# Kernel tuning notes

Measured on AMD Instinct MI355X. Metric: run time of the kernel, lower is better.

Reference implementation:

```python
import jax, jax.numpy as jnp
import numpy as np

BINS = 10


def setup_inputs() -> dict:
    key = jax.random.key(0)
    k1, k2 = jax.random.split(key)
    N, C = 4194304, 16
    inputs = jax.random.normal(k1, (N, C), dtype=jnp.float32)
    target = jax.random.randint(k2, (N,), 0, 2, dtype=jnp.int64)
    return {"inputs": inputs, "target": target}


def reference(inputs, target):
    N = inputs.shape[0]
    edges = jnp.arange(BINS + 1, dtype=inputs.dtype) / BINS  # [0, 0.1, ..., 1.0]

    # p_t = softmax(inputs)[i, target_i]
    logp = jax.nn.log_softmax(inputs, axis=1)
    p_t = jnp.take_along_axis(jnp.exp(logp), target[:, None], axis=1)[:, 0]

    # gradient norm g = |p_t - target| (detached in the original)
    g = jnp.abs(jax.lax.stop_gradient(p_t) - target.astype(inputs.dtype))

    # bin index: matches (g >= edges[i]) & (g < edges[i+1]); clip handles g == 1.0
    bin_idx = jnp.clip(jnp.searchsorted(edges, g, side="right") - 1, 0, BINS - 1)

    # per-bin counts via one scatter-add (replaces the per-bin CPU loop)
    counts = jax.ops.segment_sum(jnp.ones_like(g), bin_idx, num_segments=BINS)
    counts = jnp.maximum(counts, 1.0)  # occupied bins always have count >= 1

    # weights[i] = (N / bins) / num_in_bin(i)
    weights = (N / BINS) / counts[bin_idx]

    # weighted cross entropy, summed
    nll = -jnp.take_along_axis(logp, target[:, None], axis=1)[:, 0]
    return jnp.sum(nll * weights)
```

## Files before the change

kernel.cpp:

```cpp
#include <hip/hip_runtime.h>

#define BINS 10

__global__ __launch_bounds__(256) void ghm_main(const float* __restrict__ x,
                                                const int* __restrict__ tgt,
                                                double* __restrict__ g_sum,
                                                unsigned int* __restrict__ g_cnt,
                                                int n_rows) {
    __shared__ double s_sum[BINS];
    __shared__ unsigned int s_cnt[BINS];
    if (threadIdx.x < BINS) { s_sum[threadIdx.x] = 0.0; s_cnt[threadIdx.x] = 0u; }
    __syncthreads();

    const float edges[BINS + 1] = {0.0f, 0.1f, 0.2f, 0.3f, 0.4f, 0.5f,
                                   0.6f, 0.7f, 0.8f, 0.9f, 1.0f};

    double acc[BINS];
    unsigned int cnt[BINS];
#pragma unroll
    for (int k = 0; k < BINS; ++k) { acc[k] = 0.0; cnt[k] = 0u; }

    const int j = threadIdx.x & 3;
    const int quad = (blockIdx.x * blockDim.x + threadIdx.x) >> 2;
    const int quads_total = (gridDim.x * blockDim.x) >> 2;

    for (int row = quad; row < n_rows; row += quads_total) {
        const float4 v = ((const float4*)x)[row * 4 + j];

        float m = fmaxf(fmaxf(v.x, v.y), fmaxf(v.z, v.w));
        m = fmaxf(m, __shfl_xor(m, 1));
        m = fmaxf(m, __shfl_xor(m, 2));

        float s = expf(v.x - m) + expf(v.y - m) + expf(v.z - m) + expf(v.w - m);
        s += __shfl_xor(s, 1);
        s += __shfl_xor(s, 2);

        if (j == 0) {
            const int t = tgt[row];
            const float xt = (t == 0) ? v.x : ((t == 1) ? v.y : ((t == 2) ? v.z : v.w));
            const float logp = xt - m - logf(s);
            const float p = expf(logp);
            const float g = fabsf(p - (float)t);

            int b = 0;
#pragma unroll
            for (int k = 1; k <= BINS; ++k) b += (g >= edges[k]) ? 1 : 0;
            if (b > BINS - 1) b = BINS - 1;

            const double nll = (double)(-logp);
#pragma unroll
            for (int k = 0; k < BINS; ++k) {
                const bool h = (b == k);
                acc[k] += h ? nll : 0.0;
                cnt[k] += h ? 1u : 0u;
            }
        }
    }

#pragma unroll
    for (int k = 0; k < BINS; ++k) {
        if (cnt[k] != 0u) {
            atomicAdd(&s_cnt[k], cnt[k]);
            atomicAdd(&s_sum[k], acc[k]);
        }
    }
    __syncthreads();

    if (threadIdx.x < BINS) {
        if (s_cnt[threadIdx.x] != 0u) {
            atomicAdd(&g_cnt[threadIdx.x * 32], s_cnt[threadIdx.x]);
            atomicAdd(&g_sum[threadIdx.x * 16], s_sum[threadIdx.x]);
        }
    }
}

__global__ void ghm_final(const double* __restrict__ g_sum,
                          const unsigned int* __restrict__ g_cnt,
                          float* __restrict__ out, int n_rows) {
    if (threadIdx.x == 0 && blockIdx.x == 0) {
        const double scale = (double)n_rows / (double)BINS;
        double total = 0.0;
        for (int b = 0; b < BINS; ++b) {
            double c = (double)g_cnt[b * 32];
            if (c < 1.0) c = 1.0;
            total += g_sum[b * 16] / c;
        }
        out[0] = (float)(total * scale);
    }
}

extern "C" void kernel_launch(void* const* d_in, const int* in_sizes, int n_in,
                              void* d_out, int out_size, void* d_ws, size_t ws_size,
                              hipStream_t stream) {
    const float* x = (const float*)d_in[0];
    const int* tgt = (const int*)d_in[1];
    const int n_rows = in_sizes[1];

    double* g_sum = (double*)d_ws;
    unsigned int* g_cnt = (unsigned int*)((char*)d_ws + 2048);

    hipMemsetAsync(d_ws, 0, 4096, stream);

    const int block = 256;
    const int grid = 2048;
    ghm_main<<<grid, block, 0, stream>>>(x, tgt, g_sum, g_cnt, n_rows);
    ghm_final<<<1, 64, 0, stream>>>(g_sum, g_cnt, (float*)d_out, n_rows);
}
```

Measured before the change: 391.8 us.

## Fuse final reduction via last-block pattern, drop memset, use nontemporal loads

Replaces the memset, global atomics, and separate final kernel with per-block slot writes plus a device-wide done counter, so the last block to finish reduces all slots and writes the output. The input loads become nontemporal. This removes two extra launches and contention on the global atomics. In exchange it relies on a global counter being reset correctly and adds a serial tail reduction inside one block.

```diff
diff --git a/kernel.cpp b/kernel.cpp
--- a/kernel.cpp
+++ b/kernel.cpp
@@ -1,14 +1,22 @@
 #include <hip/hip_runtime.h>
 
 #define BINS 10
+#define GRID 2048
+#define BLOCK 256
 
-__global__ __launch_bounds__(256) void ghm_main(const float* __restrict__ x,
-                                                const int* __restrict__ tgt,
-                                                double* __restrict__ g_sum,
-                                                unsigned int* __restrict__ g_cnt,
-                                                int n_rows) {
+typedef float floatx4 __attribute__((ext_vector_type(4)));
+
+__device__ unsigned int done_ctr = 0;
+
+__global__ __launch_bounds__(BLOCK) void ghm_fused(const float* __restrict__ x,
+                                                   const int* __restrict__ tgt,
+                                                   double* __restrict__ slot_sum,
+                                                   unsigned int* __restrict__ slot_cnt,
+                                                   float* __restrict__ out,
+                                                   int n_rows) {
     __shared__ double s_sum[BINS];
     __shared__ unsigned int s_cnt[BINS];
+    __shared__ int s_last;
     if (threadIdx.x < BINS) { s_sum[threadIdx.x] = 0.0; s_cnt[threadIdx.x] = 0u; }
     __syncthreads();
 
@@ -21,23 +29,23 @@
     for (int k = 0; k < BINS; ++k) { acc[k] = 0.0; cnt[k] = 0u; }
 
     const int j = threadIdx.x & 3;
-    const int quad = (blockIdx.x * blockDim.x + threadIdx.x) >> 2;
-    const int quads_total = (gridDim.x * blockDim.x) >> 2;
+    const int quad = (blockIdx.x * BLOCK + threadIdx.x) >> 2;
+    const int quads_total = (GRID * BLOCK) >> 2;
 
     for (int row = quad; row < n_rows; row += quads_total) {
-        const float4 v = ((const float4*)x)[row * 4 + j];
+        const floatx4 v = __builtin_nontemporal_load(((const floatx4*)x) + (row * 4 + j));
 
-        float m = fmaxf(fmaxf(v.x, v.y), fmaxf(v.z, v.w));
+        float m = fmaxf(fmaxf(v[0], v[1]), fmaxf(v[2], v[3]));
         m = fmaxf(m, __shfl_xor(m, 1));
         m = fmaxf(m, __shfl_xor(m, 2));
 
-        float s = expf(v.x - m) + expf(v.y - m) + expf(v.z - m) + expf(v.w - m);
+        float s = expf(v[0] - m) + expf(v[1] - m) + expf(v[2] - m) + expf(v[3] - m);
         s += __shfl_xor(s, 1);
         s += __shfl_xor(s, 2);
 
         if (j == 0) {
             const int t = tgt[row];
-            const float xt = (t == 0) ? v.x : ((t == 1) ? v.y : ((t == 2) ? v.z : v.w));
+            const float xt = (t == 0) ? v[0] : ((t == 1) ? v[1] : ((t == 2) ? v[2] : v[3]));
             const float logp = xt - m - logf(s);
             const float p = expf(logp);
             const float g = fabsf(p - (float)t);
@@ -67,25 +75,58 @@
     __syncthreads();
 
     if (threadIdx.x < BINS) {
-        if (s_cnt[threadIdx.x] != 0u) {
-            atomicAdd(&g_cnt[threadIdx.x * 32], s_cnt[threadIdx.x]);
-            atomicAdd(&g_sum[threadIdx.x * 16], s_sum[threadIdx.x]);
+        slot_sum[threadIdx.x * GRID + blockIdx.x] = s_sum[threadIdx.x];
+        slot_cnt[threadIdx.x * GRID + blockIdx.x] = s_cnt[threadIdx.x];
+    }
+    __syncthreads();
+
+    if (threadIdx.x == 0) {
+        const unsigned int old =
+            __hip_atomic_fetch_add(&done_ctr, 1u, __ATOMIC_ACQ_REL, __HIP_MEMORY_SCOPE_AGENT);
+        s_last = (old == GRID - 1) ? 1 : 0;
+    }
+    __syncthreads();
+
+    if (s_last) {
+        double bsum[BINS];
+        unsigned int bcnt[BINS];
+#pragma unroll
+        for (int k = 0; k < BINS; ++k) { bsum[k] = 0.0; bcnt[k] = 0u; }
+        for (int i = threadIdx.x; i < GRID; i += BLOCK) {
+#pragma unroll
+            for (int k = 0; k < BINS; ++k) {
+                bsum[k] += slot_sum[k * GRID + i];
+                bcnt[k] += slot_cnt[k * GRID + i];
+            }
         }
-    }
-}
-
-__global__ void ghm_final(const double* __restrict__ g_sum,
-                          const unsigned int* __restrict__ g_cnt,
-                          float* __restrict__ out, int n_rows) {
-    if (threadIdx.x == 0 && blockIdx.x == 0) {
-        const double scale = (double)n_rows / (double)BINS;
-        double total = 0.0;
-        for (int b = 0; b < BINS; ++b) {
-            double c = (double)g_cnt[b * 32];
-            if (c < 1.0) c = 1.0;
-            total += g_sum[b * 16] / c;
+#pragma unroll
+        for (int k = 0; k < BINS; ++k) {
+            for (int off = 32; off > 0; off >>= 1) {
+                bsum[k] += __shfl_down(bsum[k], off);
+                bcnt[k] += __shfl_down(bcnt[k], off);
+            }
         }
-        out[0] = (float)(total * scale);
+        if (threadIdx.x < BINS) { s_sum[threadIdx.x] = 0.0; s_cnt[threadIdx.x] = 0u; }
+        __syncthreads();
+        if ((threadIdx.x & 63) == 0) {
+#pragma unroll
+            for (int k = 0; k < BINS; ++k) {
+                atomicAdd(&s_sum[k], bsum[k]);
+                atomicAdd(&s_cnt[k], bcnt[k]);
+            }
+        }
+        __syncthreads();
+        if (threadIdx.x == 0) {
+            const double scale = (double)n_rows / (double)BINS;
+            double total = 0.0;
+            for (int b = 0; b < BINS; ++b) {
+                double c = (double)s_cnt[b];
+                if (c < 1.0) c = 1.0;
+                total += s_sum[b] / c;
+            }
+            out[0] = (float)(total * scale);
+            __hip_atomic_store(&done_ctr, 0u, __ATOMIC_RELAXED, __HIP_MEMORY_SCOPE_AGENT);
+        }
     }
 }
 
@@ -96,13 +137,9 @@
     const int* tgt = (const int*)d_in[1];
     const int n_rows = in_sizes[1];
 
-    double* g_sum = (double*)d_ws;
-    unsigned int* g_cnt = (unsigned int*)((char*)d_ws + 2048);
+    double* slot_sum = (double*)d_ws;
+    unsigned int* slot_cnt = (unsigned int*)((char*)d_ws + BINS * GRID * sizeof(double));
 
-    hipMemsetAsync(d_ws, 0, 4096, stream);
-
-    const int block = 256;
-    const int grid = 2048;
-    ghm_main<<<grid, block, 0, stream>>>(x, tgt, g_sum, g_cnt, n_rows);
-    ghm_final<<<1, 64, 0, stream>>>(g_sum, g_cnt, (float*)d_out, n_rows);
+    ghm_fused<<<GRID, BLOCK, 0, stream>>>(x, tgt, slot_sum, slot_cnt,
+                                          (float*)d_out, n_rows);
 }
```

Result: slower. 493.9 us (+26.0%).
